# Kernel tuning notes

Hardware: AMD Instinct MI355X
Metric: run time of the kernel (lower is better)

The kernel has to match this reference:

```python
import jax, jax.numpy as jnp
import numpy as np

N = 100000      # nodes
E = 1600000     # edges (avg degree 16)
IN_CH = 128
OUT_CH = 128
MSG_DIM = 16


def setup_inputs() -> dict:
    key = jax.random.key(0)
    ks = jax.random.split(key, 9)
    x = jax.random.normal(ks[0], (N, IN_CH), dtype=jnp.float32)
    edge_index = jax.random.randint(ks[1], (2, E), 0, N, dtype=jnp.int32)
    last_update = jax.random.randint(ks[2], (N,), 0, N, dtype=jnp.int64)
    t = jax.random.uniform(ks[3], (E,), dtype=jnp.float32)
    msg = jax.random.normal(ks[4], (E, MSG_DIM), dtype=jnp.float32)
    # GCNConv weights (glorot-ish scale) and biases
    W1 = jax.random.normal(ks[5], (IN_CH, OUT_CH), dtype=jnp.float32) / np.sqrt(IN_CH)
    b1 = jnp.zeros((OUT_CH,), dtype=jnp.float32)
    W2 = jax.random.normal(ks[6], (OUT_CH, OUT_CH), dtype=jnp.float32) / np.sqrt(OUT_CH)
    b2 = jnp.zeros((OUT_CH,), dtype=jnp.float32)
    return {"x": x, "last_update": last_update, "edge_index": edge_index,
            "t": t, "msg": msg, "W1": W1, "b1": b1, "W2": W2, "b2": b2}


def _gcn_conv(x, W, b, src, dst, deg_inv_sqrt, n):
    """PyG GCNConv: out = D^{-1/2}(A+I)D^{-1/2} (x W) + b.
    src/dst already include self-loops; deg_inv_sqrt precomputed."""
    h = x @ W                                   # [N, out]
    norm = deg_inv_sqrt[src] * deg_inv_sqrt[dst]  # [E+N]
    msgs = h[src] * norm[:, None]               # gather + scale
    out = jax.ops.segment_sum(msgs, dst, num_segments=n)  # scatter-add
    return out + b


def reference(x, last_update, edge_index, t, msg, W1, b1, W2, b2):
    n = x.shape[0]
    loops = jnp.arange(n, dtype=edge_index.dtype)
    src = jnp.concatenate([edge_index[0], loops])
    dst = jnp.concatenate([edge_index[1], loops])
    # symmetric normalization degree: in-degree over dst with self-loops (>=1)
    deg = jnp.zeros((n,), x.dtype).at[dst].add(jnp.ones_like(src, x.dtype))
    deg_inv_sqrt = jax.lax.rsqrt(deg)
    h = _gcn_conv(x, W1, b1, src, dst, deg_inv_sqrt, n)
    h = jax.nn.relu(h)
    out = _gcn_conv(h, W2, b2, src, dst, deg_inv_sqrt, n)
    return out
```

## Files before the change

kernel.cpp:

```cpp
#include <hip/hip_runtime.h>
#include <hip/hip_fp16.h>
#include <stdint.h>

#define NCH 128

using half8  = __attribute__((ext_vector_type(8))) _Float16;
using floatx4 = __attribute__((ext_vector_type(4))) float;


__global__ __launch_bounds__(256) void count_kernel(const int* __restrict__ dst,
                                                    int* __restrict__ counts, int E) {
    int i = blockIdx.x * blockDim.x + threadIdx.x;
    if (i < E) atomicAdd(&counts[dst[i]], 1);
}

__global__ __launch_bounds__(1024) void scan1_kernel(const int* __restrict__ counts,
                                                     int* __restrict__ incl,
                                                     int* __restrict__ bsums, int n) {
    __shared__ int tmp[1024];
    int i = blockIdx.x * 1024 + threadIdx.x;
    int v = (i < n) ? counts[i] : 0;
    tmp[threadIdx.x] = v;
    __syncthreads();
    for (int off = 1; off < 1024; off <<= 1) {
        int t = (threadIdx.x >= off) ? tmp[threadIdx.x - off] : 0;
        __syncthreads();
        tmp[threadIdx.x] += t;
        __syncthreads();
    }
    if (i < n) incl[i] = tmp[threadIdx.x];
    if (threadIdx.x == 1023) bsums[blockIdx.x] = tmp[1023];
}

__global__ __launch_bounds__(128) void scan2_kernel(int* __restrict__ bsums, int nb) {
    __shared__ int tmp[128];
    int v = (threadIdx.x < nb) ? bsums[threadIdx.x] : 0;
    tmp[threadIdx.x] = v;
    __syncthreads();
    for (int off = 1; off < 128; off <<= 1) {
        int t = (threadIdx.x >= off) ? tmp[threadIdx.x - off] : 0;
        __syncthreads();
        tmp[threadIdx.x] += t;
        __syncthreads();
    }
    if (threadIdx.x < nb) bsums[threadIdx.x] = tmp[threadIdx.x] - v;
}

__global__ __launch_bounds__(256) void offsets_kernel(const int* __restrict__ incl,
                                                      const int* __restrict__ counts,
                                                      const int* __restrict__ bsums,
                                                      int* __restrict__ offsets,
                                                      int* __restrict__ cursor, int n) {
    int i = blockIdx.x * blockDim.x + threadIdx.x;
    if (i < n) {
        int e = incl[i] - counts[i] + bsums[i >> 10];
        offsets[i] = e;
        cursor[i] = e;
    }
}

__global__ __launch_bounds__(256) void fill_kernel(const int* __restrict__ src,
                                                   const int* __restrict__ dst,
                                                   const int* __restrict__ counts,
                                                   int* __restrict__ cursor,
                                                   unsigned int* __restrict__ emeta, int E) {
    int i = blockIdx.x * blockDim.x + threadIdx.x;
    if (i >= E) return;
    int s = src[i];
    int d = dst[i];
    unsigned int degp1 = (unsigned int)counts[s] + 1u;
    int pos = atomicAdd(&cursor[d], 1);
    emeta[pos] = (unsigned int)s | (degp1 << 17);
}


__global__ __launch_bounds__(256) void wprep_kernel(const float* __restrict__ W1,
                                                    const float* __restrict__ W2,
                                                    __half* __restrict__ Wt1,
                                                    __half* __restrict__ Wt2) {
    int b = blockIdx.x;
    const float* W = (b < 8) ? W1 : W2;
    __half* Wt     = (b < 8) ? Wt1 : Wt2;
    int c = (b & 7) * 256 + threadIdx.x;
    int p = c >> 6, lane = c & 63;
    int kc = p >> 3, ct = p & 7;
    int nn = ct * 16 + (lane & 15);
    int kbase = kc * 32 + (lane >> 4) * 8;
    half8 hv;
#pragma unroll
    for (int j = 0; j < 8; ++j)
        hv[j] = (_Float16)W[(size_t)(kbase + j) * NCH + nn];
    *(half8*)(Wt + (size_t)c * 8) = hv;
}


__global__ __launch_bounds__(256) void gemm_kernel(const float* __restrict__ A,
                                                   const __half* __restrict__ Wt,
                                                   __half* __restrict__ C, int n) {
    __shared__ float4 lds[2048];
    int t = threadIdx.x;
    for (int i = t; i < 2048; i += 256) lds[i] = ((const float4*)Wt)[i];
    __syncthreads();

    int wave = t >> 6, lane = t & 63;
    int q = lane >> 4, m16 = lane & 15;
    int rowbase = blockIdx.x * 128 + wave * 32;

    floatx4 acc[2][8];
#pragma unroll
    for (int g = 0; g < 2; ++g)
#pragma unroll
        for (int ct = 0; ct < 8; ++ct) {
            acc[g][ct][0] = 0.f; acc[g][ct][1] = 0.f;
            acc[g][ct][2] = 0.f; acc[g][ct][3] = 0.f;
        }

    const half8* bfr = (const half8*)lds;

    int ra0 = min(rowbase + m16, n - 1);
    int ra1 = min(rowbase + 16 + m16, n - 1);
    const float* pa0 = A + (size_t)ra0 * NCH;
    const float* pa1 = A + (size_t)ra1 * NCH;

#pragma unroll
    for (int kc = 0; kc < 4; ++kc) {
        int ko = kc * 32 + q * 8;
        float4 f0 = *(const float4*)(pa0 + ko);
        float4 f1 = *(const float4*)(pa0 + ko + 4);
        float4 g0 = *(const float4*)(pa1 + ko);
        float4 g1 = *(const float4*)(pa1 + ko + 4);
        half8 a0, a1;
        a0[0] = (_Float16)f0.x; a0[1] = (_Float16)f0.y;
        a0[2] = (_Float16)f0.z; a0[3] = (_Float16)f0.w;
        a0[4] = (_Float16)f1.x; a0[5] = (_Float16)f1.y;
        a0[6] = (_Float16)f1.z; a0[7] = (_Float16)f1.w;
        a1[0] = (_Float16)g0.x; a1[1] = (_Float16)g0.y;
        a1[2] = (_Float16)g0.z; a1[3] = (_Float16)g0.w;
        a1[4] = (_Float16)g1.x; a1[5] = (_Float16)g1.y;
        a1[6] = (_Float16)g1.z; a1[7] = (_Float16)g1.w;
#pragma unroll
        for (int ct = 0; ct < 8; ++ct) {
            half8 b = bfr[(kc * 8 + ct) * 64 + lane];
            acc[0][ct] = __builtin_amdgcn_mfma_f32_16x16x32_f16(a0, b, acc[0][ct], 0, 0, 0);
            acc[1][ct] = __builtin_amdgcn_mfma_f32_16x16x32_f16(a1, b, acc[1][ct], 0, 0, 0);
        }
    }

    __syncthreads();
    float* scr = (float*)lds + wave * 2048;
#pragma unroll
    for (int g = 0; g < 2; ++g) {
#pragma unroll
        for (int reg = 0; reg < 4; ++reg)
#pragma unroll
            for (int ct = 0; ct < 8; ++ct)
                scr[(q * 4 + reg) * NCH + ct * 16 + m16] = acc[g][ct][reg];
        int row0 = rowbase + g * 16;
#pragma unroll
        for (int r = 0; r < 16; ++r) {
            int row = row0 + r;
            if (row < n) {
                float2 v = *(float2*)(scr + r * NCH + lane * 2);
                __half2 hh = __floats2half2_rn(v.x, v.y);
                *(unsigned int*)(C + (size_t)row * NCH + lane * 2) = *(unsigned int*)&hh;
            }
        }
    }
}


__global__ __launch_bounds__(256) void agg_kernel(const __half2* __restrict__ hp,
                                                  const int* __restrict__ offsets,
                                                  const int* __restrict__ counts,
                                                  const unsigned int* __restrict__ emeta,
                                                  const float* __restrict__ bias,
                                                  float* __restrict__ out,
                                                  int n, int do_relu) {
    int gw = (blockIdx.x * blockDim.x + threadIdx.x) >> 6;
    int lane = threadIdx.x & 63;
    if (gw >= n) return;
    int node = gw;

    int o = offsets[node];
    int c = counts[node];
    float dn = rsqrtf((float)(c + 1));

    float2 hv = __half22float2(hp[(size_t)node * 64 + lane]);
    float w0s = dn * dn;
    float ax = hv.x * w0s, ay = hv.y * w0s;

    unsigned int m = (lane < c) ? emeta[o + lane] : 0u;
    int cc = min(c, 64);
    int j = 0;
    for (; j + 4 <= cc; j += 4) {
        unsigned int p0 = (unsigned int)__shfl((int)m, j);
        unsigned int p1 = (unsigned int)__shfl((int)m, j + 1);
        unsigned int p2 = (unsigned int)__shfl((int)m, j + 2);
        unsigned int p3 = (unsigned int)__shfl((int)m, j + 3);
        int s0 = p0 & 0x1FFFF; float w0 = rsqrtf((float)(p0 >> 17)) * dn;
        int s1 = p1 & 0x1FFFF; float w1 = rsqrtf((float)(p1 >> 17)) * dn;
        int s2 = p2 & 0x1FFFF; float w2 = rsqrtf((float)(p2 >> 17)) * dn;
        int s3 = p3 & 0x1FFFF; float w3 = rsqrtf((float)(p3 >> 17)) * dn;
        float2 v0 = __half22float2(hp[(size_t)s0 * 64 + lane]);
        float2 v1 = __half22float2(hp[(size_t)s1 * 64 + lane]);
        float2 v2 = __half22float2(hp[(size_t)s2 * 64 + lane]);
        float2 v3 = __half22float2(hp[(size_t)s3 * 64 + lane]);
        ax = fmaf(v0.x, w0, ax); ay = fmaf(v0.y, w0, ay);
        ax = fmaf(v1.x, w1, ax); ay = fmaf(v1.y, w1, ay);
        ax = fmaf(v2.x, w2, ax); ay = fmaf(v2.y, w2, ay);
        ax = fmaf(v3.x, w3, ax); ay = fmaf(v3.y, w3, ay);
    }
    for (; j < cc; ++j) {
        unsigned int p = (unsigned int)__shfl((int)m, j);
        int s = p & 0x1FFFF; float w = rsqrtf((float)(p >> 17)) * dn;
        float2 v = __half22float2(hp[(size_t)s * 64 + lane]);
        ax = fmaf(v.x, w, ax); ay = fmaf(v.y, w, ay);
    }
    for (int e = o + 64; e < o + c; ++e) {
        unsigned int p = emeta[e];
        int s = p & 0x1FFFF; float w = rsqrtf((float)(p >> 17)) * dn;
        float2 v = __half22float2(hp[(size_t)s * 64 + lane]);
        ax = fmaf(v.x, w, ax); ay = fmaf(v.y, w, ay);
    }

    float2 b = ((const float2*)bias)[lane];
    ax += b.x;
    ay += b.y;
    if (do_relu) { ax = fmaxf(ax, 0.f); ay = fmaxf(ay, 0.f); }
    float2 o2; o2.x = ax; o2.y = ay;
    ((float2*)out)[(size_t)node * 64 + lane] = o2;
}


extern "C" void kernel_launch(void* const* d_in, const int* in_sizes, int n_in,
                              void* d_out, int out_size, void* d_ws, size_t ws_size,
                              hipStream_t stream) {
    const float* x  = (const float*)d_in[0];
    const int* edge = (const int*)d_in[2];
    const float* W1 = (const float*)d_in[5];
    const float* b1 = (const float*)d_in[6];
    const float* W2 = (const float*)d_in[7];
    const float* b2 = (const float*)d_in[8];

    int n = in_sizes[0] / NCH;
    int E = in_sizes[2] / 2;
    const int* srcp = edge;
    const int* dstp = edge + E;

    char* ws = (char*)d_ws;
    int*   counts  = (int*)ws;   ws += (size_t)n * 4;
    int*   incl    = (int*)ws;   ws += (size_t)n * 4;
    int*   offsets = (int*)ws;   ws += (size_t)n * 4;
    int*   cursor  = (int*)ws;   ws += (size_t)n * 4;
    int*   bsums   = (int*)ws;   ws += 1024;
    uintptr_t pw = ((uintptr_t)ws + 255) & ~(uintptr_t)255;
    __half* Wt1 = (__half*)pw;   pw += 2048 * 16;
    __half* Wt2 = (__half*)pw;   pw += 2048 * 16;
    unsigned int* emeta = (unsigned int*)pw; pw += (size_t)E * 4;
    uintptr_t p = (pw + 255) & ~(uintptr_t)255;
    __half* h = (__half*)p;
    float* out = (float*)d_out;

    hipMemsetAsync(counts, 0, (size_t)n * 4, stream);

    wprep_kernel<<<16, 256, 0, stream>>>(W1, W2, Wt1, Wt2);
    count_kernel<<<(E + 255) / 256, 256, 0, stream>>>(dstp, counts, E);

    int nb = (n + 1023) / 1024;
    scan1_kernel<<<nb, 1024, 0, stream>>>(counts, incl, bsums, n);
    scan2_kernel<<<1, 128, 0, stream>>>(bsums, nb);
    offsets_kernel<<<(n + 255) / 256, 256, 0, stream>>>(incl, counts, bsums, offsets, cursor, n);
    fill_kernel<<<(E + 255) / 256, 256, 0, stream>>>(srcp, dstp, counts, cursor, emeta, E);

    int gemm_blocks = (n + 127) / 128;
    int agg_blocks  = (n + 3) / 4;

    gemm_kernel<<<gemm_blocks, 256, 0, stream>>>(x, Wt1, h, n);
    agg_kernel<<<agg_blocks, 256, 0, stream>>>((const __half2*)h, offsets, counts, emeta, b1, out, n, 1);
    gemm_kernel<<<gemm_blocks, 256, 0, stream>>>(out, Wt2, h, n);
    agg_kernel<<<agg_blocks, 256, 0, stream>>>((const __half2*)h, offsets, counts, emeta, b2, out, n, 0);
}
```

Baseline: 497.8 us.

## Merge independent prep kernels and store layer-1 activations in fp16

Folds the weight-prep work into the degree-count kernel, and the CSR fill into the first GEMM launch, so that independent work shares one launch. The first aggregation now writes its ReLU output as fp16 into the output buffer, and a new fp16-input GEMM reads it. This halves the traffic for the intermediate activations and drops the fp32-to-fp16 conversion in the second GEMM. The cost is extra precision loss from rounding the intermediate activations to fp16, and fill blocks competing with GEMM blocks for the GPU.

After: 487.6 us. -2.1%, faster.

```diff
diff --git a/kernel.cpp b/kernel.cpp
--- a/kernel.cpp
+++ b/kernel.cpp
@@ -8,10 +8,30 @@
 using floatx4 = __attribute__((ext_vector_type(4))) float;
 
 
-__global__ __launch_bounds__(256) void count_kernel(const int* __restrict__ dst,
-                                                    int* __restrict__ counts, int E) {
-    int i = blockIdx.x * blockDim.x + threadIdx.x;
-    if (i < E) atomicAdd(&counts[dst[i]], 1);
+__global__ __launch_bounds__(256) void count_wprep_kernel(const int* __restrict__ dst,
+                                                          int* __restrict__ counts, int E,
+                                                          const float* __restrict__ W1,
+                                                          const float* __restrict__ W2,
+                                                          __half* __restrict__ Wt1,
+                                                          __half* __restrict__ Wt2) {
+    int b = blockIdx.x;
+    if (b < 16) {
+        const float* W = (b < 8) ? W1 : W2;
+        __half* Wt     = (b < 8) ? Wt1 : Wt2;
+        int c = (b & 7) * 256 + threadIdx.x;
+        int p = c >> 6, lane = c & 63;
+        int kc = p >> 3, ct = p & 7;
+        int nn = ct * 16 + (lane & 15);
+        int kbase = kc * 32 + (lane >> 4) * 8;
+        half8 hv;
+#pragma unroll
+        for (int j = 0; j < 8; ++j)
+            hv[j] = (_Float16)W[(size_t)(kbase + j) * NCH + nn];
+        *(half8*)(Wt + (size_t)c * 8) = hv;
+    } else {
+        int i = (b - 16) * 256 + threadIdx.x;
+        if (i < E) atomicAdd(&counts[dst[i]], 1);
+    }
 }
 
 __global__ __launch_bounds__(1024) void scan1_kernel(const int* __restrict__ counts,
@@ -59,52 +79,37 @@
     }
 }
 
-__global__ __launch_bounds__(256) void fill_kernel(const int* __restrict__ src,
-                                                   const int* __restrict__ dst,
-                                                   const int* __restrict__ counts,
-                                                   int* __restrict__ cursor,
-                                                   unsigned int* __restrict__ emeta, int E) {
-    int i = blockIdx.x * blockDim.x + threadIdx.x;
-    if (i >= E) return;
-    int s = src[i];
-    int d = dst[i];
-    unsigned int degp1 = (unsigned int)counts[s] + 1u;
-    int pos = atomicAdd(&cursor[d], 1);
-    emeta[pos] = (unsigned int)s | (degp1 << 17);
-}
-
-
-__global__ __launch_bounds__(256) void wprep_kernel(const float* __restrict__ W1,
-                                                    const float* __restrict__ W2,
-                                                    __half* __restrict__ Wt1,
-                                                    __half* __restrict__ Wt2) {
-    int b = blockIdx.x;
-    const float* W = (b < 8) ? W1 : W2;
-    __half* Wt     = (b < 8) ? Wt1 : Wt2;
-    int c = (b & 7) * 256 + threadIdx.x;
-    int p = c >> 6, lane = c & 63;
-    int kc = p >> 3, ct = p & 7;
-    int nn = ct * 16 + (lane & 15);
-    int kbase = kc * 32 + (lane >> 4) * 8;
-    half8 hv;
-#pragma unroll
-    for (int j = 0; j < 8; ++j)
-        hv[j] = (_Float16)W[(size_t)(kbase + j) * NCH + nn];
-    *(half8*)(Wt + (size_t)c * 8) = hv;
-}
-
-
-__global__ __launch_bounds__(256) void gemm_kernel(const float* __restrict__ A,
-                                                   const __half* __restrict__ Wt,
-                                                   __half* __restrict__ C, int n) {
+
+__global__ __launch_bounds__(256) void fill_gemm_kernel(const float* __restrict__ A,
+                                                        const __half* __restrict__ Wt,
+                                                        __half* __restrict__ C, int n,
+                                                        int gemm_blocks,
+                                                        const int* __restrict__ src,
+                                                        const int* __restrict__ dst,
+                                                        const int* __restrict__ counts,
+                                                        int* __restrict__ cursor,
+                                                        unsigned int* __restrict__ emeta,
+                                                        int E) {
     __shared__ float4 lds[2048];
+    int bid = blockIdx.x;
+    if (bid >= gemm_blocks) {
+        int i = (bid - gemm_blocks) * 256 + threadIdx.x;
+        if (i < E) {
+            int s = src[i];
+            int d = dst[i];
+            unsigned int degp1 = (unsigned int)counts[s] + 1u;
+            int pos = atomicAdd(&cursor[d], 1);
+            emeta[pos] = (unsigned int)s | (degp1 << 17);
+        }
+        return;
+    }
     int t = threadIdx.x;
     for (int i = t; i < 2048; i += 256) lds[i] = ((const float4*)Wt)[i];
     __syncthreads();
 
     int wave = t >> 6, lane = t & 63;
     int q = lane >> 4, m16 = lane & 15;
-    int rowbase = blockIdx.x * 128 + wave * 32;
+    int rowbase = bid * 128 + wave * 32;
 
     floatx4 acc[2][8];
 #pragma unroll
@@ -169,13 +174,77 @@
 }
 
 
+__global__ __launch_bounds__(256) void gemm_h_kernel(const __half* __restrict__ A,
+                                                     const __half* __restrict__ Wt,
+                                                     __half* __restrict__ C, int n) {
+    __shared__ float4 lds[2048];
+    int t = threadIdx.x;
+    for (int i = t; i < 2048; i += 256) lds[i] = ((const float4*)Wt)[i];
+    __syncthreads();
+
+    int wave = t >> 6, lane = t & 63;
+    int q = lane >> 4, m16 = lane & 15;
+    int rowbase = blockIdx.x * 128 + wave * 32;
+
+    floatx4 acc[2][8];
+#pragma unroll
+    for (int g = 0; g < 2; ++g)
+#pragma unroll
+        for (int ct = 0; ct < 8; ++ct) {
+            acc[g][ct][0] = 0.f; acc[g][ct][1] = 0.f;
+            acc[g][ct][2] = 0.f; acc[g][ct][3] = 0.f;
+        }
+
+    const half8* bfr = (const half8*)lds;
+
+    int ra0 = min(rowbase + m16, n - 1);
+    int ra1 = min(rowbase + 16 + m16, n - 1);
+    const _Float16* pa0 = (const _Float16*)A + (size_t)ra0 * NCH;
+    const _Float16* pa1 = (const _Float16*)A + (size_t)ra1 * NCH;
+
+#pragma unroll
+    for (int kc = 0; kc < 4; ++kc) {
+        int ko = kc * 32 + q * 8;
+        half8 a0 = *(const half8*)(pa0 + ko);
+        half8 a1 = *(const half8*)(pa1 + ko);
+#pragma unroll
+        for (int ct = 0; ct < 8; ++ct) {
+            half8 b = bfr[(kc * 8 + ct) * 64 + lane];
+            acc[0][ct] = __builtin_amdgcn_mfma_f32_16x16x32_f16(a0, b, acc[0][ct], 0, 0, 0);
+            acc[1][ct] = __builtin_amdgcn_mfma_f32_16x16x32_f16(a1, b, acc[1][ct], 0, 0, 0);
+        }
+    }
+
+    __syncthreads();
+    float* scr = (float*)lds + wave * 2048;
+#pragma unroll
+    for (int g = 0; g < 2; ++g) {
+#pragma unroll
+        for (int reg = 0; reg < 4; ++reg)
+#pragma unroll
+            for (int ct = 0; ct < 8; ++ct)
+                scr[(q * 4 + reg) * NCH + ct * 16 + m16] = acc[g][ct][reg];
+        int row0 = rowbase + g * 16;
+#pragma unroll
+        for (int r = 0; r < 16; ++r) {
+            int row = row0 + r;
+            if (row < n) {
+                float2 v = *(float2*)(scr + r * NCH + lane * 2);
+                __half2 hh = __floats2half2_rn(v.x, v.y);
+                *(unsigned int*)(C + (size_t)row * NCH + lane * 2) = *(unsigned int*)&hh;
+            }
+        }
+    }
+}
+
+
 __global__ __launch_bounds__(256) void agg_kernel(const __half2* __restrict__ hp,
                                                   const int* __restrict__ offsets,
                                                   const int* __restrict__ counts,
                                                   const unsigned int* __restrict__ emeta,
                                                   const float* __restrict__ bias,
-                                                  float* __restrict__ out,
-                                                  int n, int do_relu) {
+                                                  void* __restrict__ outp,
+                                                  int n, int do_relu, int out_fp16) {
     int gw = (blockIdx.x * blockDim.x + threadIdx.x) >> 6;
     int lane = threadIdx.x & 63;
     if (gw >= n) return;
@@ -227,8 +296,13 @@
     ax += b.x;
     ay += b.y;
     if (do_relu) { ax = fmaxf(ax, 0.f); ay = fmaxf(ay, 0.f); }
-    float2 o2; o2.x = ax; o2.y = ay;
-    ((float2*)out)[(size_t)node * 64 + lane] = o2;
+    if (out_fp16) {
+        __half2 hh = __floats2half2_rn(ax, ay);
+        ((__half2*)outp)[(size_t)node * 64 + lane] = hh;
+    } else {
+        float2 o2; o2.x = ax; o2.y = ay;
+        ((float2*)outp)[(size_t)node * 64 + lane] = o2;
+    }
 }
 
 
@@ -260,23 +334,26 @@
     uintptr_t p = (pw + 255) & ~(uintptr_t)255;
     __half* h = (__half*)p;
     float* out = (float*)d_out;
+    __half* a1 = (__half*)d_out;
 
     hipMemsetAsync(counts, 0, (size_t)n * 4, stream);
 
-    wprep_kernel<<<16, 256, 0, stream>>>(W1, W2, Wt1, Wt2);
-    count_kernel<<<(E + 255) / 256, 256, 0, stream>>>(dstp, counts, E);
+    int count_blocks = (E + 255) / 256;
+    count_wprep_kernel<<<16 + count_blocks, 256, 0, stream>>>(dstp, counts, E, W1, W2, Wt1, Wt2);
 
     int nb = (n + 1023) / 1024;
     scan1_kernel<<<nb, 1024, 0, stream>>>(counts, incl, bsums, n);
     scan2_kernel<<<1, 128, 0, stream>>>(bsums, nb);
     offsets_kernel<<<(n + 255) / 256, 256, 0, stream>>>(incl, counts, bsums, offsets, cursor, n);
-    fill_kernel<<<(E + 255) / 256, 256, 0, stream>>>(srcp, dstp, counts, cursor, emeta, E);
 
     int gemm_blocks = (n + 127) / 128;
+    int fill_blocks = (E + 255) / 256;
     int agg_blocks  = (n + 3) / 4;
 
-    gemm_kernel<<<gemm_blocks, 256, 0, stream>>>(x, Wt1, h, n);
-    agg_kernel<<<agg_blocks, 256, 0, stream>>>((const __half2*)h, offsets, counts, emeta, b1, out, n, 1);
-    gemm_kernel<<<gemm_blocks, 256, 0, stream>>>(out, Wt2, h, n);
-    agg_kernel<<<agg_blocks, 256, 0, stream>>>((const __half2*)h, offsets, counts, emeta, b2, out, n, 0);
-}
+    fill_gemm_kernel<<<gemm_blocks + fill_blocks, 256, 0, stream>>>(
+        x, Wt1, h, n, gemm_blocks, srcp, dstp, counts, cursor, emeta, E);
+
+    agg_kernel<<<agg_blocks, 256, 0, stream>>>((const __half2*)h, offsets, counts, emeta, b1, a1, n, 1, 1);
+    gemm_h_kernel<<<gemm_blocks, 256, 0, stream>>>(a1, Wt2, h, n);
+    agg_kernel<<<agg_blocks, 256, 0, stream>>>((const __half2*)h, offsets, counts, emeta, b2, out, n, 0, 0);
+}
```
